# Kernel optimization log

Measured on AMD Instinct MI355X. Metric: run time of the kernel, lower is better.

## Reference

```python
import jax, jax.numpy as jnp
import numpy as np

N_NODES = 100000
N_EDGES = 3200000
INPUT_DIM = 128
HIDDEN = 64


def spmm(row, col, vals, x, n):
    # out[i] = sum_{e: row[e]==i} vals[e] * x[col[e]]  -- COO SpMM via gather + segment_sum
    msgs = vals[:, None] * x[col]  # [E, F]
    return jax.ops.segment_sum(msgs, row, num_segments=n)


def setup_inputs() -> dict:
    key = jax.random.key(0)
    ks = jax.random.split(key, 12)
    embeddings = jax.random.normal(ks[0], (N_NODES, INPUT_DIM), dtype=jnp.float32)
    norm_degrees = jax.random.uniform(ks[1], (N_NODES, 1), dtype=jnp.float32)
    seed_mask = (jax.random.uniform(ks[2], (N_NODES, 1)) < 0.05).astype(jnp.float32)
    adj_row = jax.random.randint(ks[3], (N_EDGES,), 0, N_NODES, dtype=jnp.int32)
    adj_col = jax.random.randint(ks[4], (N_EDGES,), 0, N_NODES, dtype=jnp.int32)
    adj_vals = jax.random.uniform(ks[5], (N_EDGES,), dtype=jnp.float32)
    d_in = INPUT_DIM + 2
    # Linear params (torch Linear: y = x @ W.T + b); store W as [in, out]
    W1 = jax.random.normal(ks[6], (d_in, HIDDEN), dtype=jnp.float32) / np.sqrt(d_in)
    b1 = jnp.zeros((HIDDEN,), dtype=jnp.float32)
    W2 = jax.random.normal(ks[7], (HIDDEN, HIDDEN), dtype=jnp.float32) / np.sqrt(HIDDEN)
    b2 = jnp.zeros((HIDDEN,), dtype=jnp.float32)
    W_out = jax.random.normal(ks[8], (HIDDEN, 1), dtype=jnp.float32) / np.sqrt(HIDDEN)
    b_out = jnp.zeros((1,), dtype=jnp.float32)
    return {
        "embeddings": embeddings, "norm_degrees": norm_degrees, "seed_mask": seed_mask,
        "adj_row": adj_row, "adj_col": adj_col, "adj_vals": adj_vals,
        "W1": W1, "b1": b1, "W2": W2, "b2": b2, "W_out": W_out, "b_out": b_out,
    }


def reference(embeddings, norm_degrees, seed_mask, adj_row, adj_col, adj_vals,
              W1, b1, W2, b2, W_out, b_out):
    n = embeddings.shape[0]
    x = jnp.concatenate([embeddings, norm_degrees, seed_mask], axis=1)  # [N, input_dim+2]
    x = x @ W1 + b1                       # conv1
    x = jax.nn.relu(spmm(adj_row, adj_col, adj_vals, x, n))
    x = x @ W2 + b2                       # conv2
    x = jax.nn.relu(spmm(adj_row, adj_col, adj_vals, x, n))
    graph_rep = jnp.sum(x, axis=0)        # [HIDDEN]
    return graph_rep @ W_out + b_out      # [1]
```

## Files before the change

### kernel.cpp

```cpp
#include <hip/hip_runtime.h>
#include <hip/hip_bf16.h>

#define HID 64
#define IN_EMB 128
#define IN_DIM 130
#define ROWS_PER_BKT 512
#define LOG_RPB 9
#define MAX_BKT 256
#define PART_CHUNK 8192
#define SLOT_E 18432
#define ASTR 168
#define BSTR 72
#define RPB 32
#define ECAP 2048

typedef __hip_bfloat16 bf16;
typedef __attribute__((ext_vector_type(8))) short bf16x8;
typedef __attribute__((ext_vector_type(4))) float fx4;
typedef __attribute__((ext_vector_type(2))) float fx2;

__device__ __forceinline__ short f2bfs(float f) {
  __hip_bfloat16 h = __float2bfloat16(f);
  return *(reinterpret_cast<short*>(&h));
}
__device__ __forceinline__ int pk_fp8x4(float a, float b, float c, float d) {
  int v = __builtin_amdgcn_cvt_pk_fp8_f32(a, b, 0, false);
  v = __builtin_amdgcn_cvt_pk_fp8_f32(c, d, v, true);
  return v;
}
__device__ __forceinline__ unsigned char f2fp8(float x) {
  return (unsigned char)(__builtin_amdgcn_cvt_pk_fp8_f32(x, x, 0, false) & 0xFF);
}

__global__ __launch_bounds__(1024) void bscan_kernel(const int* __restrict__ bcnt,
                                                     int* __restrict__ bstart,
                                                     int* __restrict__ row_ptr,
                                                     int n, int nbkt) {
  __shared__ int s[1024];
  const int t = threadIdx.x;
  const int v = (t < nbkt) ? bcnt[t] : 0;
  s[t] = v;
  __syncthreads();
  for (int off = 1; off < 1024; off <<= 1) {
    int u = (t >= off) ? s[t - off] : 0;
    __syncthreads();
    s[t] += u;
    __syncthreads();
  }
  if (t < nbkt) bstart[t] = s[t] - v;
  if (t == 0) { bstart[nbkt] = s[1023]; row_ptr[n] = s[1023]; }
}

__global__ __launch_bounds__(512) void partition_kernel(
    const int* __restrict__ row, const int* __restrict__ col,
    const float* __restrict__ vals, int* __restrict__ bcur,
    int2* __restrict__ tmp, int nE) {
  __shared__ int h[MAX_BKT];
  __shared__ int cur[MAX_BKT];
  const int t = threadIdx.x;
  const int base = blockIdx.x * PART_CHUNK;
  for (int i = t; i < MAX_BKT; i += 512) h[i] = 0;
  __syncthreads();
  for (int kk = t; kk < PART_CHUNK / 4; kk += 512) {
    int e0 = base + kk * 4;
    if (e0 + 3 < nE) {
      int4 r4 = ((const int4*)row)[(base >> 2) + kk];
      atomicAdd(&h[r4.x >> LOG_RPB], 1);
      atomicAdd(&h[r4.y >> LOG_RPB], 1);
      atomicAdd(&h[r4.z >> LOG_RPB], 1);
      atomicAdd(&h[r4.w >> LOG_RPB], 1);
    } else {
      for (int j = 0; j < 4; ++j) {
        int e = e0 + j;
        if (e < nE) atomicAdd(&h[row[e] >> LOG_RPB], 1);
      }
    }
  }
  __syncthreads();
  for (int b = t; b < MAX_BKT; b += 512)
    if (h[b] > 0) cur[b] = b * SLOT_E + atomicAdd(&bcur[b], h[b]);
  __syncthreads();
  for (int kk = t; kk < PART_CHUNK / 4; kk += 512) {
    int e0 = base + kk * 4;
    if (e0 + 3 < nE) {
      int4 r4 = ((const int4*)row)[(base >> 2) + kk];
      int4 c4 = ((const int4*)col)[(base >> 2) + kk];
      float4 v4 = ((const float4*)vals)[(base >> 2) + kk];
      int rr[4] = {r4.x, r4.y, r4.z, r4.w};
      int cc[4] = {c4.x, c4.y, c4.z, c4.w};
      float vv[4] = {v4.x, v4.y, v4.z, v4.w};
#pragma unroll
      for (int j = 0; j < 4; ++j) {
        int b = rr[j] >> LOG_RPB;
        int p = atomicAdd(&cur[b], 1);
        if (p - b * SLOT_E < SLOT_E)
          tmp[p] = make_int2(cc[j] | ((rr[j] & (ROWS_PER_BKT - 1)) << 20),
                             __float_as_int(vv[j]));
      }
    } else {
      for (int j = 0; j < 4; ++j) {
        int e = e0 + j;
        if (e < nE) {
          int r = row[e];
          int b = r >> LOG_RPB;
          int p = atomicAdd(&cur[b], 1);
          if (p - b * SLOT_E < SLOT_E)
            tmp[p] = make_int2(col[e] | ((r & (ROWS_PER_BKT - 1)) << 20),
                               __float_as_int(vals[e]));
        }
      }
    }
  }
}

__global__ __launch_bounds__(512) void bucket_sort_kernel(
    const int* __restrict__ bstart, const int2* __restrict__ tmp,
    int2* __restrict__ ce, int* __restrict__ row_ptr, int n) {
  __shared__ int rcnt[ROWS_PER_BKT];
  __shared__ int rpos[ROWS_PER_BKT];
  __shared__ int sc[ROWS_PER_BKT];
  const int t = threadIdx.x;
  const int b = blockIdx.x;
  const int start = bstart[b];
  const int len   = bstart[b + 1] - start;
  const int2* ts = tmp + (size_t)b * SLOT_E;
  rcnt[t] = 0;
  __syncthreads();
  const int* keys = (const int*)ts;
  for (int i = t; i < len; i += 512)
    atomicAdd(&rcnt[((unsigned)keys[2 * i]) >> 20], 1);
  __syncthreads();
  sc[t] = rcnt[t];
  __syncthreads();
  for (int off = 1; off < ROWS_PER_BKT; off <<= 1) {
    int u = (t >= off) ? sc[t - off] : 0;
    __syncthreads();
    sc[t] += u;
    __syncthreads();
  }
  {
    int ex = sc[t] - rcnt[t];
    int gpos = start + ex;
    rpos[t] = gpos;
    int gr = b * ROWS_PER_BKT + t;
    if (gr < n) row_ptr[gr] = gpos;
  }
  __syncthreads();
  for (int i = t; i < len; i += 512) {
    int2 e = ts[i];
    int p = atomicAdd(&rpos[((unsigned)e.x) >> 20], 1);
    ce[p] = make_int2(e.x & 0xFFFFF, e.y);
  }
}

__global__ __launch_bounds__(256) void lin1_kernel(
    const float* __restrict__ emb, const float* __restrict__ deg,
    const float* __restrict__ seed, const float* __restrict__ W1,
    const float* __restrict__ b1, unsigned char* __restrict__ out, int n) {
  __shared__ short sB[64 * ASTR];
  const int t = threadIdx.x;
  const int base = blockIdx.x * 256;

  for (int idx = t; idx < 64 * 160; idx += 256) {
    int k = idx >> 6, nn = idx & 63;
    float v = (k < IN_DIM) ? W1[k * HID + nn] : 0.f;
    sB[nn * ASTR + k] = f2bfs(v);
  }
  __syncthreads();

  const int lane = t & 63, w = t >> 6;
  const int nl = lane & 15, q = lane >> 4;
  const short* pB = &sB[nl * ASTR + q * 8];
  const float bias0 = b1[nl], bias1 = b1[16 + nl],
              bias2 = b1[32 + nl], bias3 = b1[48 + nl];

#pragma unroll
  for (int tile = 0; tile < 4; ++tile) {
    const int g64 = base + tile * 64;
    const int anode = g64 + w * 16 + nl;
    bf16x8 afr[5];
    if (anode < n) {
      const float4* ep = (const float4*)(emb + (size_t)anode * IN_EMB);
#pragma unroll
      for (int kt = 0; kt < 4; ++kt) {
        float4 v0 = ep[q * 2 + kt * 8];
        float4 v1 = ep[q * 2 + 1 + kt * 8];
        bf16x8 a;
        a[0] = f2bfs(v0.x); a[1] = f2bfs(v0.y); a[2] = f2bfs(v0.z); a[3] = f2bfs(v0.w);
        a[4] = f2bfs(v1.x); a[5] = f2bfs(v1.y); a[6] = f2bfs(v1.z); a[7] = f2bfs(v1.w);
        afr[kt] = a;
      }
      bf16x8 a4 = {0, 0, 0, 0, 0, 0, 0, 0};
      if (q == 0) { a4[0] = f2bfs(deg[anode]); a4[1] = f2bfs(seed[anode]); }
      afr[4] = a4;
    } else {
#pragma unroll
      for (int kt = 0; kt < 5; ++kt) afr[kt] = (bf16x8){0, 0, 0, 0, 0, 0, 0, 0};
    }

    fx4 ac0 = {0.f, 0.f, 0.f, 0.f}, ac1 = ac0, ac2 = ac0, ac3 = ac0;
#pragma unroll
    for (int kt = 0; kt < 5; ++kt) {
      bf16x8 b0  = *(const bf16x8*)(pB + kt * 32);
      bf16x8 b1v = *(const bf16x8*)(pB + 16 * ASTR + kt * 32);
      bf16x8 b2v = *(const bf16x8*)(pB + 32 * ASTR + kt * 32);
      bf16x8 b3v = *(const bf16x8*)(pB + 48 * ASTR + kt * 32);
      ac0 = __builtin_amdgcn_mfma_f32_16x16x32_bf16(afr[kt], b0,  ac0, 0, 0, 0);
      ac1 = __builtin_amdgcn_mfma_f32_16x16x32_bf16(afr[kt], b1v, ac1, 0, 0, 0);
      ac2 = __builtin_amdgcn_mfma_f32_16x16x32_bf16(afr[kt], b2v, ac2, 0, 0, 0);
      ac3 = __builtin_amdgcn_mfma_f32_16x16x32_bf16(afr[kt], b3v, ac3, 0, 0, 0);
    }
#pragma unroll
    for (int r = 0; r < 4; ++r) {
      int node = g64 + w * 16 + q * 4 + r;
      if (node < n) {
        unsigned char* o = out + ((size_t)node << 6);
        o[nl]      = f2fp8(ac0[r] + bias0);
        o[16 + nl] = f2fp8(ac1[r] + bias1);
        o[32 + nl] = f2fp8(ac2[r] + bias2);
        o[48 + nl] = f2fp8(ac3[r] + bias3);
      }
    }
  }
}

#define GLD(ev, u)                                                            \
  const uint2 u = *(const uint2*)(xp + (((size_t)(unsigned)(ev)) << 6) + 8 * fl);
#define GMAD(ev, u)                                                           \
  {                                                                           \
    const float v = __int_as_float((int)((ev) >> 32));                        \
    const fx2 v2 = {v, v};                                                    \
    a0 += v2 * __builtin_amdgcn_cvt_pk_f32_fp8(u.x, false);                   \
    a1 += v2 * __builtin_amdgcn_cvt_pk_f32_fp8(u.x, true);                    \
    a2 += v2 * __builtin_amdgcn_cvt_pk_f32_fp8(u.y, false);                   \
    a3 += v2 * __builtin_amdgcn_cvt_pk_f32_fp8(u.y, true);                    \
  }
#define GMAD_P(ev, u, ok)                                                     \
  {                                                                           \
    const float v = (ok) ? __int_as_float((int)((ev) >> 32)) : 0.f;           \
    const fx2 v2 = {v, v};                                                    \
    a0 += v2 * __builtin_amdgcn_cvt_pk_f32_fp8(u.x, false);                   \
    a1 += v2 * __builtin_amdgcn_cvt_pk_f32_fp8(u.x, true);                    \
    a2 += v2 * __builtin_amdgcn_cvt_pk_f32_fp8(u.y, false);                   \
    a3 += v2 * __builtin_amdgcn_cvt_pk_f32_fp8(u.y, true);                    \
  }

#define SPMM_STAGE_EDGES                                                      \
  const unsigned long long* cep = (const unsigned long long*)ce;              \
  const int r0blk = blockIdx.x * RPB;                                         \
  const int bstartE = row_ptr[r0blk];                                         \
  const int bendE = row_ptr[(r0blk + RPB < n) ? (r0blk + RPB) : n];           \
  const int cnt = min(bendE - bstartE, ECAP);                                 \
  for (int ii = threadIdx.x; ii < cnt; ii += 256)                             \
    eb[ii] = __builtin_nontemporal_load(cep + bstartE + ii);                  \
  __syncthreads();

#define SPMM_GATHER_BODY                                                      \
  const int i0r = row_ptr[r];                                                 \
  const int endr = row_ptr[r + 1];                                            \
  const int lend = endr - bstartE;                                            \
  if (lend <= cnt) {                                                          \
    int i = i0r - bstartE;                                                    \
    for (; i + 4 <= lend; i += 4) {                                           \
      unsigned long long e0 = eb[i];                                          \
      unsigned long long e1 = eb[i + 1];                                      \
      unsigned long long e2 = eb[i + 2];                                      \
      unsigned long long e3 = eb[i + 3];                                      \
      GLD(e0, u0); GLD(e1, u1); GLD(e2, u2); GLD(e3, u3);                     \
      GMAD(e0, u0); GMAD(e1, u1); GMAD(e2, u2); GMAD(e3, u3);                 \
    }                                                                         \
    if (i < lend) {                                                           \
      const int last = lend - 1;                                              \
      bool k1 = i + 1 < lend, k2 = i + 2 < lend, k3 = i + 3 < lend;           \
      unsigned long long e0 = eb[i];                                          \
      unsigned long long e1 = eb[k1 ? i + 1 : last];                          \
      unsigned long long e2 = eb[k2 ? i + 2 : last];                          \
      unsigned long long e3 = eb[k3 ? i + 3 : last];                          \
      GLD(e0, u0); GLD(e1, u1); GLD(e2, u2); GLD(e3, u3);                     \
      GMAD(e0, u0); GMAD_P(e1, u1, k1);                                       \
      GMAD_P(e2, u2, k2); GMAD_P(e3, u3, k3);                                 \
    }                                                                         \
  } else {                                                                    \
    int i = i0r;                                                              \
    for (; i + 4 <= endr; i += 4) {                                           \
      unsigned long long e0 = __builtin_nontemporal_load(cep + i);            \
      unsigned long long e1 = __builtin_nontemporal_load(cep + i + 1);        \
      unsigned long long e2 = __builtin_nontemporal_load(cep + i + 2);        \
      unsigned long long e3 = __builtin_nontemporal_load(cep + i + 3);        \
      GLD(e0, u0); GLD(e1, u1); GLD(e2, u2); GLD(e3, u3);                     \
      GMAD(e0, u0); GMAD(e1, u1); GMAD(e2, u2); GMAD(e3, u3);                 \
    }                                                                         \
    if (i < endr) {                                                           \
      const int last = endr - 1;                                              \
      bool k1 = i + 1 < endr, k2 = i + 2 < endr, k3 = i + 3 < endr;           \
      unsigned long long e0 = cep[i];                                         \
      unsigned long long e1 = cep[k1 ? i + 1 : last];                         \
      unsigned long long e2 = cep[k2 ? i + 2 : last];                         \
      unsigned long long e3 = cep[k3 ? i + 3 : last];                         \
      GLD(e0, u0); GLD(e1, u1); GLD(e2, u2); GLD(e3, u3);                     \
      GMAD(e0, u0); GMAD_P(e1, u1, k1);                                       \
      GMAD_P(e2, u2, k2); GMAD_P(e3, u3, k3);                                 \
    }                                                                         \
  }

__global__ __launch_bounds__(256) void spmm_csr_kernel(
    const int* __restrict__ row_ptr, const int2* __restrict__ ce,
    const unsigned char* __restrict__ x, unsigned char* __restrict__ y, int n) {
  __shared__ unsigned long long eb[ECAP];
  const int fl = threadIdx.x & 7;
  const int r = blockIdx.x * RPB + (threadIdx.x >> 3);
  const unsigned char* xp = x;
  SPMM_STAGE_EDGES
  if (r < n) {
    fx2 a0 = {0.f, 0.f}, a1 = a0, a2 = a0, a3 = a0;
    SPMM_GATHER_BODY
    int lo = pk_fp8x4(fmaxf(a0.x, 0.f), fmaxf(a0.y, 0.f),
                      fmaxf(a1.x, 0.f), fmaxf(a1.y, 0.f));
    int hi = pk_fp8x4(fmaxf(a2.x, 0.f), fmaxf(a2.y, 0.f),
                      fmaxf(a3.x, 0.f), fmaxf(a3.y, 0.f));
    *(int2*)(y + ((size_t)r << 6) + 8 * fl) = make_int2(lo, hi);
  }
}

__global__ __launch_bounds__(256) void lin2_kernel(
    const unsigned char* __restrict__ yin, const float* __restrict__ W2,
    const float* __restrict__ b2, unsigned char* __restrict__ xout, int n) {
  __shared__ short sB[64 * BSTR];
  const int t = threadIdx.x;
  const int base = blockIdx.x * 256;
  for (int idx = t; idx < 64 * 64; idx += 256) {
    int k = idx >> 6, nn = idx & 63;
    sB[nn * BSTR + k] = f2bfs(W2[k * HID + nn]);
  }
  __syncthreads();

  const int lane = t & 63, w = t >> 6;
  const int nl = lane & 15, q = lane >> 4;
  const short* pB = &sB[nl * BSTR + q * 8];
  const float bias0 = b2[nl], bias1 = b2[16 + nl],
              bias2 = b2[32 + nl], bias3 = b2[48 + nl];

#pragma unroll
  for (int tile = 0; tile < 4; ++tile) {
    const int g64 = base + tile * 64;
    const int anode = g64 + w * 16 + nl;
    const unsigned char* xg = yin + (((size_t)anode) << 6) + q * 8;
    fx4 ac0 = {0.f, 0.f, 0.f, 0.f}, ac1 = ac0, ac2 = ac0, ac3 = ac0;
#pragma unroll
    for (int kt = 0; kt < 2; ++kt) {
      uint2 u8 = (anode < n) ? *(const uint2*)(xg + kt * 32) : make_uint2(0u, 0u);
      fx2 f0 = __builtin_amdgcn_cvt_pk_f32_fp8(u8.x, false);
      fx2 f1 = __builtin_amdgcn_cvt_pk_f32_fp8(u8.x, true);
      fx2 f2 = __builtin_amdgcn_cvt_pk_f32_fp8(u8.y, false);
      fx2 f3 = __builtin_amdgcn_cvt_pk_f32_fp8(u8.y, true);
      bf16x8 a;
      a[0] = f2bfs(f0.x); a[1] = f2bfs(f0.y); a[2] = f2bfs(f1.x); a[3] = f2bfs(f1.y);
      a[4] = f2bfs(f2.x); a[5] = f2bfs(f2.y); a[6] = f2bfs(f3.x); a[7] = f2bfs(f3.y);
      bf16x8 b0  = *(const bf16x8*)(pB + kt * 32);
      bf16x8 b1v = *(const bf16x8*)(pB + 16 * BSTR + kt * 32);
      bf16x8 b2v = *(const bf16x8*)(pB + 32 * BSTR + kt * 32);
      bf16x8 b3v = *(const bf16x8*)(pB + 48 * BSTR + kt * 32);
      ac0 = __builtin_amdgcn_mfma_f32_16x16x32_bf16(a, b0,  ac0, 0, 0, 0);
      ac1 = __builtin_amdgcn_mfma_f32_16x16x32_bf16(a, b1v, ac1, 0, 0, 0);
      ac2 = __builtin_amdgcn_mfma_f32_16x16x32_bf16(a, b2v, ac2, 0, 0, 0);
      ac3 = __builtin_amdgcn_mfma_f32_16x16x32_bf16(a, b3v, ac3, 0, 0, 0);
    }
#pragma unroll
    for (int r = 0; r < 4; ++r) {
      int node = g64 + w * 16 + q * 4 + r;
      if (node < n) {
        unsigned char* o = xout + ((size_t)node << 6);
        o[nl]      = f2fp8(ac0[r] + bias0);
        o[16 + nl] = f2fp8(ac1[r] + bias1);
        o[32 + nl] = f2fp8(ac2[r] + bias2);
        o[48 + nl] = f2fp8(ac3[r] + bias3);
      }
    }
  }
}

__global__ __launch_bounds__(256) void spmm2_fused_kernel(
    const int* __restrict__ row_ptr, const int2* __restrict__ ce,
    const unsigned char* __restrict__ x, const float* __restrict__ Wout,
    float* __restrict__ partials, int n) {
  __shared__ unsigned long long eb[ECAP];
  const int fl = threadIdx.x & 7;
  const int r = blockIdx.x * RPB + (threadIdx.x >> 3);
  const unsigned char* xp = x;
  SPMM_STAGE_EDGES
  float wpart = 0.f;
  if (r < n) {
    fx2 a0 = {0.f, 0.f}, a1 = a0, a2 = a0, a3 = a0;
    SPMM_GATHER_BODY
    const float4 wv0 = ((const float4*)Wout)[2 * fl];
    const float4 wv1 = ((const float4*)Wout)[2 * fl + 1];
    wpart = fmaxf(a0.x, 0.f) * wv0.x + fmaxf(a0.y, 0.f) * wv0.y
          + fmaxf(a1.x, 0.f) * wv0.z + fmaxf(a1.y, 0.f) * wv0.w
          + fmaxf(a2.x, 0.f) * wv1.x + fmaxf(a2.y, 0.f) * wv1.y
          + fmaxf(a3.x, 0.f) * wv1.z + fmaxf(a3.y, 0.f) * wv1.w;
  }
  for (int off = 32; off; off >>= 1) wpart += __shfl_down(wpart, off, 64);
  __shared__ float part[4];
  const int lane = threadIdx.x & 63;
  if (lane == 0) part[threadIdx.x >> 6] = wpart;
  __syncthreads();
  if (threadIdx.x == 0)
    partials[blockIdx.x] = part[0] + part[1] + part[2] + part[3];
}

__global__ __launch_bounds__(1024) void reduce_kernel(
    const float* __restrict__ partials, const float* __restrict__ bout,
    float* __restrict__ out, int m) {
  const int t = threadIdx.x;
  float s = 0.f;
  const int m4 = m >> 2;
  for (int i = t; i < m4; i += 1024) {
    float4 v = ((const float4*)partials)[i];
    s += v.x + v.y + v.z + v.w;
  }
  if (t < (m & 3)) s += partials[(m & ~3) + t];
  for (int off = 32; off; off >>= 1) s += __shfl_down(s, off, 64);
  __shared__ float wsum[16];
  if ((t & 63) == 0) wsum[t >> 6] = s;
  __syncthreads();
  if (t == 0) {
    float tot = bout[0];
    for (int w = 0; w < 16; ++w) tot += wsum[w];
    out[0] = tot;
  }
}

extern "C" void kernel_launch(void* const* d_in, const int* in_sizes, int n_in,
                              void* d_out, int out_size, void* d_ws, size_t ws_size,
                              hipStream_t stream) {
  const float* emb  = (const float*)d_in[0];
  const float* deg  = (const float*)d_in[1];
  const float* seed = (const float*)d_in[2];
  const int*   row  = (const int*)d_in[3];
  const int*   col  = (const int*)d_in[4];
  const float* vals = (const float*)d_in[5];
  const float* W1   = (const float*)d_in[6];
  const float* b1   = (const float*)d_in[7];
  const float* W2   = (const float*)d_in[8];
  const float* b2   = (const float*)d_in[9];
  const float* Wout = (const float*)d_in[10];
  const float* bout = (const float*)d_in[11];
  float* out = (float*)d_out;

  const int n  = in_sizes[0] / IN_EMB;
  const int nE = in_sizes[3];
  const int nbkt = (n + ROWS_PER_BKT - 1) / ROWS_PER_BKT;

  const int lin_blocks  = (n + 255) / 256;
  const int row_blocks  = (n + RPB - 1) / RPB;
  const int part_blocks = (nE + PART_CHUNK - 1) / PART_CHUNK;

  char* ws = (char*)d_ws;
  int2* ce   = (int2*)ws;  ws += (size_t)nE * sizeof(int2);
  char* tmpb = ws;
  int2* tmp  = (int2*)ws;  ws += (size_t)nbkt * SLOT_E * sizeof(int2);
  unsigned char* xb = (unsigned char*)ws;  ws += ((size_t)n * HID + 255) & ~255ULL;
  int* row_ptr = (int*)ws; ws += ((size_t)(n + 1) * 4 + 255) & ~255ULL;
  int* bcur    = (int*)ws; ws += ((size_t)nbkt * 4 + 255) & ~255ULL;
  int* bstart  = (int*)ws; ws += ((size_t)(nbkt + 1) * 4 + 255) & ~255ULL;
  float* partials = (float*)ws;
  unsigned char* xa = (unsigned char*)tmpb;
  unsigned char* ya = (unsigned char*)(tmpb + (8u << 20));

  hipMemsetAsync(bcur, 0, (size_t)nbkt * sizeof(int), stream);
  partition_kernel<<<part_blocks, 512, 0, stream>>>(row, col, vals, bcur, tmp, nE);
  bscan_kernel<<<1, 1024, 0, stream>>>(bcur, bstart, row_ptr, n, nbkt);
  bucket_sort_kernel<<<nbkt, 512, 0, stream>>>(bstart, tmp, ce, row_ptr, n);

  lin1_kernel<<<lin_blocks, 256, 0, stream>>>(emb, deg, seed, W1, b1, xa, n);
  spmm_csr_kernel<<<row_blocks, 256, 0, stream>>>(row_ptr, ce, xa, ya, n);
  lin2_kernel<<<lin_blocks, 256, 0, stream>>>(ya, W2, b2, xb, n);
  spmm2_fused_kernel<<<row_blocks, 256, 0, stream>>>(row_ptr, ce, xb, Wout, partials, n);
  reduce_kernel<<<1, 1024, 0, stream>>>(partials, bout, out, row_blocks);
}
```

Baseline: 297.2 us.

## Stage partitioned edges in LDS for coalesced bucket writes

The partition kernel now computes a local prefix sum over bucket counts, scatters each chunk's edges into a shared-memory buffer grouped by bucket, and then writes them out to the global bucket slots in contiguous runs. The aim is to replace scattered 8-byte global stores with mostly coalesced ones. The chunk size is halved to fit the staging buffer in LDS, which doubles the number of blocks and the global atomics on bucket counters. It also adds an extra block-wide scan and barrier phase.

```diff
diff --git a/kernel.cpp b/kernel.cpp
--- a/kernel.cpp
+++ b/kernel.cpp
@@ -7,7 +7,7 @@
 #define ROWS_PER_BKT 512
 #define LOG_RPB 9
 #define MAX_BKT 256
-#define PART_CHUNK 8192
+#define PART_CHUNK 4096
 #define SLOT_E 18432
 #define ASTR 168
 #define BSTR 72
@@ -55,11 +55,18 @@
     const int* __restrict__ row, const int* __restrict__ col,
     const float* __restrict__ vals, int* __restrict__ bcur,
     int2* __restrict__ tmp, int nE) {
+  __shared__ int2 lbuf[PART_CHUNK];
+  __shared__ unsigned char lbid[PART_CHUNK];
   __shared__ int h[MAX_BKT];
-  __shared__ int cur[MAX_BKT];
+  __shared__ int sc[MAX_BKT];
+  __shared__ int lofs[MAX_BKT + 1];
+  __shared__ int lcur[MAX_BKT];
+  __shared__ int gbase[MAX_BKT];
   const int t = threadIdx.x;
   const int base = blockIdx.x * PART_CHUNK;
-  for (int i = t; i < MAX_BKT; i += 512) h[i] = 0;
+  const int cntE = min(PART_CHUNK, nE - base);
+
+  if (t < MAX_BKT) h[t] = 0;
   __syncthreads();
   for (int kk = t; kk < PART_CHUNK / 4; kk += 512) {
     int e0 = base + kk * 4;
@@ -77,8 +84,21 @@
     }
   }
   __syncthreads();
-  for (int b = t; b < MAX_BKT; b += 512)
-    if (h[b] > 0) cur[b] = b * SLOT_E + atomicAdd(&bcur[b], h[b]);
+  if (t < MAX_BKT) sc[t] = h[t];
+  __syncthreads();
+  for (int off = 1; off < MAX_BKT; off <<= 1) {
+    int u = (t < MAX_BKT && t >= off) ? sc[t - off] : 0;
+    __syncthreads();
+    if (t < MAX_BKT) sc[t] += u;
+    __syncthreads();
+  }
+  if (t < MAX_BKT) {
+    int ex = sc[t] - h[t];
+    lofs[t] = ex;
+    lcur[t] = ex;
+    if (h[t] > 0) gbase[t] = t * SLOT_E + atomicAdd(&bcur[t], h[t]);
+  }
+  if (t == MAX_BKT - 1) lofs[MAX_BKT] = sc[t];
   __syncthreads();
   for (int kk = t; kk < PART_CHUNK / 4; kk += 512) {
     int e0 = base + kk * 4;
@@ -92,10 +112,10 @@
 #pragma unroll
       for (int j = 0; j < 4; ++j) {
         int b = rr[j] >> LOG_RPB;
-        int p = atomicAdd(&cur[b], 1);
-        if (p - b * SLOT_E < SLOT_E)
-          tmp[p] = make_int2(cc[j] | ((rr[j] & (ROWS_PER_BKT - 1)) << 20),
-                             __float_as_int(vv[j]));
+        int p = atomicAdd(&lcur[b], 1);
+        lbuf[p] = make_int2(cc[j] | ((rr[j] & (ROWS_PER_BKT - 1)) << 20),
+                            __float_as_int(vv[j]));
+        lbid[p] = (unsigned char)b;
       }
     } else {
       for (int j = 0; j < 4; ++j) {
@@ -103,13 +123,20 @@
         if (e < nE) {
           int r = row[e];
           int b = r >> LOG_RPB;
-          int p = atomicAdd(&cur[b], 1);
-          if (p - b * SLOT_E < SLOT_E)
-            tmp[p] = make_int2(col[e] | ((r & (ROWS_PER_BKT - 1)) << 20),
-                               __float_as_int(vals[e]));
+          int p = atomicAdd(&lcur[b], 1);
+          lbuf[p] = make_int2(col[e] | ((r & (ROWS_PER_BKT - 1)) << 20),
+                              __float_as_int(vals[e]));
+          lbid[p] = (unsigned char)b;
         }
       }
     }
+  }
+  __syncthreads();
+  for (int i = t; i < cntE; i += 512) {
+    int b = lbid[i];
+    int off = i - lofs[b];
+    int g = gbase[b] + off;
+    if (g - b * SLOT_E < SLOT_E) tmp[g] = lbuf[i];
   }
 }
 
```

Result: no change. 292.1 us (-1.7%).
